# Performance work log

Hardware: AMD Instinct MI355X
Metric: run time of the kernel (lower is better)

The kernel has to match this reference:

```python
import jax, jax.numpy as jnp
import numpy as np

TH = 0.95      # hardcoded entropy threshold in the 'normal' branch of forward
EPS = 1e-12    # eps added to distances in get_entropy

B, C, K, D = 262144, 1000, 3, 64  # batch, num_classes, num_centers, feature_dim


def setup_inputs() -> dict:
    key = jax.random.key(0)
    k1, k2, k3 = jax.random.split(key, 3)
    x = jax.random.normal(k1, (B, D), dtype=jnp.float32)
    labels = jax.random.randint(k2, (B,), 0, C, dtype=jnp.int32)
    centers = jax.random.normal(k3, (C, K, D), dtype=jnp.float32)  # nn.Parameter, init_way='normal'
    return {"x": x, "labels": labels, "centers": centers}


def reference(x, labels, centers):
    # The torch code builds the full [B, C, K] distance tensor and then gathers the
    # label's class; only the positive-class distances are ever used, so we gather
    # the centers first (same math, no [B, C, K, D] / [B, C, K] blowup).
    c = centers[labels]                                   # [B, K, D]
    pos = jnp.sum((x[:, None, :] - c) ** 2, axis=-1)      # [B, K] squared distances

    min_pos = jnp.min(pos, axis=1)                        # [B]

    # two smallest distances, ascending (== sorted_values[:2])
    two_smallest = -jax.lax.top_k(-pos, 2)[0]             # [B, 2]
    d = two_smallest + EPS
    p = d[:, 0] / (d[:, 0] + d[:, 1])                     # p <= 0.5
    entropy = -(p * jnp.log2(p) + (1.0 - p) * jnp.log2(1.0 - p))
    mask = entropy <= TH                                  # mask[i]=False when entropy > 0.95 (num_centers>1)

    loss1 = jnp.mean(min_pos)
    cnt = jnp.sum(mask.astype(min_pos.dtype))
    loss2 = jnp.sum(jnp.where(mask, min_pos, 0.0)) / cnt  # == min_pos[mask].mean()
    return loss1, loss2
```

## Files before the change

### kernel.cpp

```cpp
#include <hip/hip_runtime.h>


#define TH   0.95f
#define EPSF 1e-12f
#define NBLK 2048
#define BLK  256
#define ITERS 8

typedef float f4 __attribute__((ext_vector_type(4)));

__global__ __launch_bounds__(BLK) void mp_main(
    const float* __restrict__ x,
    const int*   __restrict__ labels,
    const float* __restrict__ centers,
    float*       __restrict__ partials)
{
    const int tid  = threadIdx.x;
    const int lane = tid & 63;
    const int wave = tid >> 6;
    const int sub  = lane & 15;
    const int rsub = lane >> 4;

    const f4* __restrict__ x4 = (const f4*)x;
    const f4* __restrict__ c4 = (const f4*)centers;

    const int rowbase = blockIdx.x * (16 * ITERS) + wave * 4 + rsub;

    int labs[ITERS];
    #pragma unroll
    for (int t = 0; t < ITERS; ++t)
        labs[t] = __builtin_nontemporal_load(&labels[rowbase + t * 16]);

    float s1 = 0.f, s2 = 0.f, sc = 0.f;

    #pragma unroll
    for (int t = 0; t < ITERS; ++t) {
        const int row = rowbase + t * 16;

        const f4 xv = __builtin_nontemporal_load(&x4[row * 16 + sub]);

        const f4* cb = c4 + labs[t] * 48 + sub;
        const f4 cv0 = cb[0];
        const f4 cv1 = cb[16];
        const f4 cv2 = cb[32];

        f4 d;
        d = xv - cv0;
        float a0 = d.x * d.x + d.y * d.y + d.z * d.z + d.w * d.w;
        d = xv - cv1;
        float a1 = d.x * d.x + d.y * d.y + d.z * d.z + d.w * d.w;
        d = xv - cv2;
        float a2 = d.x * d.x + d.y * d.y + d.z * d.z + d.w * d.w;

        #pragma unroll
        for (int m = 1; m <= 8; m <<= 1) {
            a0 += __shfl_xor(a0, m);
            a1 += __shfl_xor(a1, m);
            a2 += __shfl_xor(a2, m);
        }

        const float mn  = fminf(a0, fminf(a1, a2));
        const float mx  = fmaxf(a0, fmaxf(a1, a2));
        const float mid = a0 + a1 + a2 - mn - mx;

        const float d0 = mn + EPSF, d1 = mid + EPSF;
        const float p  = d0 / (d0 + d1);
        const float q  = 1.f - p;
        const float ent = -(p * __log2f(p) + q * __log2f(q));
        const float msk = (ent <= TH) ? 1.f : 0.f;

        const float w = (sub == 0) ? 1.f : 0.f;
        s1 += w * mn;
        s2 += w * msk * mn;
        sc += w * msk;
    }

    #pragma unroll
    for (int m = 1; m <= 32; m <<= 1) {
        s1 += __shfl_xor(s1, m);
        s2 += __shfl_xor(s2, m);
        sc += __shfl_xor(sc, m);
    }

    __shared__ float red[3][4];
    if (lane == 0) { red[0][wave] = s1; red[1][wave] = s2; red[2][wave] = sc; }
    __syncthreads();
    if (tid == 0) {
        partials[blockIdx.x]            = red[0][0] + red[0][1] + red[0][2] + red[0][3];
        partials[NBLK + blockIdx.x]     = red[1][0] + red[1][1] + red[1][2] + red[1][3];
        partials[2 * NBLK + blockIdx.x] = red[2][0] + red[2][1] + red[2][2] + red[2][3];
    }
}

__global__ __launch_bounds__(BLK) void mp_final(
    const float* __restrict__ partials, float* __restrict__ out, float invB)
{
    const int tid  = threadIdx.x;
    const int lane = tid & 63;
    const int wave = tid >> 6;

    float s1 = 0.f, s2 = 0.f, sc = 0.f;
    for (int i = tid; i < NBLK; i += BLK) {
        s1 += partials[i];
        s2 += partials[NBLK + i];
        sc += partials[2 * NBLK + i];
    }
    #pragma unroll
    for (int m = 1; m <= 32; m <<= 1) {
        s1 += __shfl_xor(s1, m);
        s2 += __shfl_xor(s2, m);
        sc += __shfl_xor(sc, m);
    }
    __shared__ float red[3][4];
    if (lane == 0) { red[0][wave] = s1; red[1][wave] = s2; red[2][wave] = sc; }
    __syncthreads();
    if (tid == 0) {
        float t1 = red[0][0] + red[0][1] + red[0][2] + red[0][3];
        float t2 = red[1][0] + red[1][1] + red[1][2] + red[1][3];
        float t3 = red[2][0] + red[2][1] + red[2][2] + red[2][3];
        out[0] = t1 * invB;
        out[1] = t2 / t3;
    }
}

extern "C" void kernel_launch(void* const* d_in, const int* in_sizes, int n_in,
                              void* d_out, int out_size, void* d_ws, size_t ws_size,
                              hipStream_t stream) {
    const float* x       = (const float*)d_in[0];
    const int*   labels  = (const int*)d_in[1];
    const float* centers = (const float*)d_in[2];
    float* out      = (float*)d_out;
    float* partials = (float*)d_ws;
    const int B = in_sizes[1];

    mp_main<<<NBLK, BLK, 0, stream>>>(x, labels, centers, partials);
    mp_final<<<1, BLK, 0, stream>>>(partials, out, 1.0f / (float)B);
}
```

Before: 111.8 us.

## Fuse final reduction via last-block atomic counter and use DPP row sums

```diff
diff --git a/kernel.cpp b/kernel.cpp
--- a/kernel.cpp
+++ b/kernel.cpp
@@ -9,11 +9,26 @@
 
 typedef float f4 __attribute__((ext_vector_type(4)));
 
+template <int CTRL>
+__device__ __forceinline__ float dpp_ror_add(float v) {
+    int t = __builtin_amdgcn_mov_dpp(__float_as_int(v), CTRL, 0xf, 0xf, true);
+    return v + __int_as_float(t);
+}
+__device__ __forceinline__ float row16_sum(float v) {
+    v = dpp_ror_add<0x128>(v);
+    v = dpp_ror_add<0x124>(v);
+    v = dpp_ror_add<0x122>(v);
+    v = dpp_ror_add<0x121>(v);
+    return v;
+}
+
 __global__ __launch_bounds__(BLK) void mp_main(
     const float* __restrict__ x,
     const int*   __restrict__ labels,
     const float* __restrict__ centers,
-    float*       __restrict__ partials)
+    float*       __restrict__ partials,
+    float*       __restrict__ out,
+    float invB)
 {
     const int tid  = threadIdx.x;
     const int lane = tid & 63;
@@ -52,12 +67,9 @@
         d = xv - cv2;
         float a2 = d.x * d.x + d.y * d.y + d.z * d.z + d.w * d.w;
 
-        #pragma unroll
-        for (int m = 1; m <= 8; m <<= 1) {
-            a0 += __shfl_xor(a0, m);
-            a1 += __shfl_xor(a1, m);
-            a2 += __shfl_xor(a2, m);
-        }
+        a0 = row16_sum(a0);
+        a1 = row16_sum(a1);
+        a2 = row16_sum(a2);
 
         const float mn  = fminf(a0, fminf(a1, a2));
         const float mx  = fmaxf(a0, fmaxf(a1, a2));
@@ -83,43 +95,46 @@
     }
 
     __shared__ float red[3][4];
+    __shared__ int lastFlag;
     if (lane == 0) { red[0][wave] = s1; red[1][wave] = s2; red[2][wave] = sc; }
     __syncthreads();
+
+    unsigned int* counter = (unsigned int*)&partials[3 * NBLK];
     if (tid == 0) {
-        partials[blockIdx.x]            = red[0][0] + red[0][1] + red[0][2] + red[0][3];
-        partials[NBLK + blockIdx.x]     = red[1][0] + red[1][1] + red[1][2] + red[1][3];
-        partials[2 * NBLK + blockIdx.x] = red[2][0] + red[2][1] + red[2][2] + red[2][3];
+        float p1 = red[0][0] + red[0][1] + red[0][2] + red[0][3];
+        float p2 = red[1][0] + red[1][1] + red[1][2] + red[1][3];
+        float p3 = red[2][0] + red[2][1] + red[2][2] + red[2][3];
+        __hip_atomic_store(&partials[blockIdx.x],            p1, __ATOMIC_RELAXED, __HIP_MEMORY_SCOPE_AGENT);
+        __hip_atomic_store(&partials[NBLK + blockIdx.x],     p2, __ATOMIC_RELAXED, __HIP_MEMORY_SCOPE_AGENT);
+        __hip_atomic_store(&partials[2 * NBLK + blockIdx.x], p3, __ATOMIC_RELAXED, __HIP_MEMORY_SCOPE_AGENT);
+        unsigned old = __hip_atomic_fetch_add(counter, 1u, __ATOMIC_ACQ_REL, __HIP_MEMORY_SCOPE_AGENT);
+        lastFlag = (old == NBLK - 1);
     }
-}
+    __syncthreads();
 
-__global__ __launch_bounds__(BLK) void mp_final(
-    const float* __restrict__ partials, float* __restrict__ out, float invB)
-{
-    const int tid  = threadIdx.x;
-    const int lane = tid & 63;
-    const int wave = tid >> 6;
-
-    float s1 = 0.f, s2 = 0.f, sc = 0.f;
-    for (int i = tid; i < NBLK; i += BLK) {
-        s1 += partials[i];
-        s2 += partials[NBLK + i];
-        sc += partials[2 * NBLK + i];
-    }
-    #pragma unroll
-    for (int m = 1; m <= 32; m <<= 1) {
-        s1 += __shfl_xor(s1, m);
-        s2 += __shfl_xor(s2, m);
-        sc += __shfl_xor(sc, m);
-    }
-    __shared__ float red[3][4];
-    if (lane == 0) { red[0][wave] = s1; red[1][wave] = s2; red[2][wave] = sc; }
-    __syncthreads();
-    if (tid == 0) {
-        float t1 = red[0][0] + red[0][1] + red[0][2] + red[0][3];
-        float t2 = red[1][0] + red[1][1] + red[1][2] + red[1][3];
-        float t3 = red[2][0] + red[2][1] + red[2][2] + red[2][3];
-        out[0] = t1 * invB;
-        out[1] = t2 / t3;
+    if (lastFlag) {
+        float t1 = 0.f, t2 = 0.f, t3 = 0.f;
+        for (int i = tid; i < NBLK; i += BLK) {
+            t1 += __hip_atomic_load(&partials[i],            __ATOMIC_RELAXED, __HIP_MEMORY_SCOPE_AGENT);
+            t2 += __hip_atomic_load(&partials[NBLK + i],     __ATOMIC_RELAXED, __HIP_MEMORY_SCOPE_AGENT);
+            t3 += __hip_atomic_load(&partials[2 * NBLK + i], __ATOMIC_RELAXED, __HIP_MEMORY_SCOPE_AGENT);
+        }
+        #pragma unroll
+        for (int m = 1; m <= 32; m <<= 1) {
+            t1 += __shfl_xor(t1, m);
+            t2 += __shfl_xor(t2, m);
+            t3 += __shfl_xor(t3, m);
+        }
+        __syncthreads();
+        if (lane == 0) { red[0][wave] = t1; red[1][wave] = t2; red[2][wave] = t3; }
+        __syncthreads();
+        if (tid == 0) {
+            float f1 = red[0][0] + red[0][1] + red[0][2] + red[0][3];
+            float f2 = red[1][0] + red[1][1] + red[1][2] + red[1][3];
+            float f3 = red[2][0] + red[2][1] + red[2][2] + red[2][3];
+            out[0] = f1 * invB;
+            out[1] = f2 / f3;
+        }
     }
 }
 
@@ -133,6 +148,6 @@
     float* partials = (float*)d_ws;
     const int B = in_sizes[1];
 
-    mp_main<<<NBLK, BLK, 0, stream>>>(x, labels, centers, partials);
-    mp_final<<<1, BLK, 0, stream>>>(partials, out, 1.0f / (float)B);
+    hipMemsetAsync((void*)(partials + 3 * NBLK), 0, sizeof(unsigned int), stream);
+    mp_main<<<NBLK, BLK, 0, stream>>>(x, labels, centers, partials, out, 1.0f / (float)B);
 }
```

Measured after the change: 205.1 us. +83.5%, slower.
